# Kernel tuning notes

Hardware: AMD Instinct MI355X
Metric: run time of the kernel (lower is better)

Reference implementation:

```python
import jax, jax.numpy as jnp
import numpy as np

DIM_IN = 1024
DIM_Q = 1024
DIM_K = 1024
DIM_V = 1024
HEADS = 16

def setup_inputs() -> dict:
    key = jax.random.key(0)
    ks = jax.random.split(key, 5)
    s = 1.0 / np.sqrt(DIM_IN)
    return {
        "x": jax.random.normal(ks[0], (2, 2048, DIM_IN), dtype=jnp.float32),
        "Wq": jax.random.uniform(ks[1], (DIM_IN, DIM_Q), jnp.float32, -s, s),
        "Wk": jax.random.uniform(ks[2], (DIM_IN, DIM_K), jnp.float32, -s, s),
        "Wv": jax.random.uniform(ks[3], (DIM_IN, DIM_V), jnp.float32, -s, s),
        "Wo": jax.random.uniform(ks[4], (DIM_V, DIM_V), jnp.float32, -1.0/np.sqrt(DIM_V), 1.0/np.sqrt(DIM_V)),
    }

def reference(x, Wq, Wk, Wv, Wo):
    B, S, _ = x.shape
    H = HEADS
    q = (x @ Wq).reshape(B, S, H, DIM_Q // H).transpose(0, 2, 1, 3)  # [B,H,S,dq]
    k = (x @ Wk).reshape(B, S, H, DIM_K // H).transpose(0, 2, 1, 3)
    v = (x @ Wv).reshape(B, S, H, DIM_V // H).transpose(0, 2, 1, 3)
    scores = jnp.einsum("bhsd,bhtd->bhst", q, k)  # no pre-softmax scaling (as in source)
    # NOTE: source divides by sqrt(dim_q) AFTER softmax — replicated faithfully.
    attn = jax.nn.softmax(scores, axis=-1) / jnp.sqrt(jnp.float32(DIM_Q))
    out = jnp.einsum("bhst,bhtd->bhsd", attn, v)  # [B,H,S,dv]
    out = out.transpose(0, 2, 1, 3).reshape(B, S, DIM_V)
    return out @ Wo
```

## Files before the change

### kernel.cpp

```cpp
#include <hip/hip_runtime.h>
#include <hip/hip_bf16.h>


typedef __attribute__((ext_vector_type(8))) short bf16x8;
typedef __attribute__((ext_vector_type(4))) short short4v;
typedef __attribute__((ext_vector_type(4))) float f32x4;

typedef const __attribute__((address_space(1))) void gvoid_t;
typedef __attribute__((address_space(3))) void svoid_t;
#define GLDS16(g, l) \
  __builtin_amdgcn_global_load_lds((gvoid_t*)(g), (svoid_t*)(l), 16, 0, 0)

#define MFMA16(a, b, c) __builtin_amdgcn_mfma_f32_16x16x32_bf16((a), (b), (c), 0, 0, 0)

#if defined(__has_builtin)
#if __has_builtin(__builtin_amdgcn_exp2f)
#define EXP2(x) __builtin_amdgcn_exp2f(x)
#else
#define EXP2(x) exp2f(x)
#endif
#else
#define EXP2(x) exp2f(x)
#endif

#define LOG2E 1.4426950408889634f
#define NSHIFT 17.312340490667561f

static __device__ __forceinline__ short f2bf(float f) {
  __hip_bfloat16 h = __float2bfloat16(f);
  short s;
  __builtin_memcpy(&s, &h, 2);
  return s;
}

static __device__ __forceinline__ unsigned pack2bf(float lo, float hi) {
  float2 t; t.x = lo; t.y = hi;
  __hip_bfloat162 h2 = __float22bfloat162_rn(t);
  unsigned u;
  __builtin_memcpy(&u, &h2, 4);
  return u;
}

__global__ __launch_bounds__(256) void prep(const float* __restrict__ x,
                                            const float* __restrict__ Wq,
                                            const float* __restrict__ Wk,
                                            const float* __restrict__ Wv,
                                            const float* __restrict__ Wo,
                                            short* __restrict__ xb,
                                            short* __restrict__ wqkvt,
                                            short* __restrict__ wot) {
  __shared__ float tile[64][65];
  int bid = blockIdx.x;
  int tid = threadIdx.x;
  if (bid < 2048) {
    int i = bid * 256 + tid;
    const float4* p = (const float4*)(x + (size_t)i * 8);
    float4 a = p[0], b = p[1];
    bf16x8 o;
    o[0] = f2bf(a.x); o[1] = f2bf(a.y); o[2] = f2bf(a.z); o[3] = f2bf(a.w);
    o[4] = f2bf(b.x); o[5] = f2bf(b.y); o[6] = f2bf(b.z); o[7] = f2bf(b.w);
    *(bf16x8*)(xb + (size_t)i * 8) = o;
    return;
  }
  bid -= 2048;
  int mat = bid >> 8;
  int t = bid & 255;
  int tn = (t & 15) * 64;
  int tk = (t >> 4) * 64;
  const float* src = (mat == 0) ? Wq : (mat == 1) ? Wk : (mat == 2) ? Wv : Wo;
  short* dst = (mat < 3) ? (wqkvt + (size_t)mat * 1024 * 1024) : wot;

  int c4 = (tid & 15) * 4;
#pragma unroll
  for (int it = 0; it < 4; ++it) {
    int r = (tid >> 4) + it * 16;
    float4 v = *(const float4*)(src + (size_t)(tk + r) * 1024 + tn + c4);
    tile[r][c4 + 0] = v.x; tile[r][c4 + 1] = v.y;
    tile[r][c4 + 2] = v.z; tile[r][c4 + 3] = v.w;
  }
  __syncthreads();
  int n = tid >> 2;
  int kc = (tid & 3) * 16;
  bf16x8 o0, o1;
#pragma unroll
  for (int j = 0; j < 8; ++j) {
    o0[j] = f2bf(tile[kc + j][n]);
    o1[j] = f2bf(tile[kc + 8 + j][n]);
  }
  *(bf16x8*)(dst + (size_t)(tn + n) * 1024 + tk + kc) = o0;
  *(bf16x8*)(dst + (size_t)(tn + n) * 1024 + tk + kc + 8) = o1;
}

__global__ __launch_bounds__(512, 4) void gemm_qkv(const short* __restrict__ A,
                                                   const short* __restrict__ Bt,
                                                   short* __restrict__ qk,
                                                   short* __restrict__ vt) {
  constexpr int K = 1024;
  __shared__ short As[2][128 * 64];
  __shared__ short Bs[2][192 * 64];
  const int tid = threadIdx.x;
  const int lane = tid & 63;
  const int w = tid >> 6;
  const int lr = lane & 15, lg = lane >> 4;
  const int m0 = blockIdx.y * 128, n0 = blockIdx.x * 192;
  const int wm = (w >> 2) * 64, wn = (w & 3) * 48;

  auto stage = [&](int kt, int bb) {
#pragma unroll
    for (int it = 0; it < 2; ++it) {
      int id = it * 512 + tid;
      int row = id >> 3, c = id & 7;
      int sc = c ^ (row & 7);
      GLDS16(A + (size_t)(m0 + row) * K + kt + sc * 8, &As[bb][0] + id * 8);
    }
#pragma unroll
    for (int it = 0; it < 3; ++it) {
      int id = it * 512 + tid;
      int row = id >> 3, c = id & 7;
      int sc = c ^ (row & 7);
      GLDS16(Bt + (size_t)(n0 + row) * K + kt + sc * 8, &Bs[bb][0] + id * 8);
    }
  };

  f32x4 acc[4][3] = {};

  stage(0, 0);
  __syncthreads();

  int cur = 0;
  for (int kt = 0; kt < K; kt += 64) {
    if (kt + 64 < K) stage(kt + 64, cur ^ 1);
    const short* Ab = &As[cur][0];
    const short* Bb = &Bs[cur][0];
#pragma unroll
    for (int kk2 = 0; kk2 < 2; ++kk2) {
      int cw = kk2 * 4 + lg;
      bf16x8 bfr[3];
#pragma unroll
      for (int ni = 0; ni < 3; ++ni) {
        int row = wn + ni * 16 + lr;
        bfr[ni] = *(const bf16x8*)(Bb + row * 64 + ((cw ^ (row & 7)) * 8));
      }
      __builtin_amdgcn_s_setprio(1);
#pragma unroll
      for (int mi = 0; mi < 4; ++mi) {
        int row = wm + mi * 16 + lr;
        bf16x8 af = *(const bf16x8*)(Ab + row * 64 + ((cw ^ (row & 7)) * 8));
#pragma unroll
        for (int ni = 0; ni < 3; ++ni)
          acc[mi][ni] = MFMA16(af, bfr[ni], acc[mi][ni]);
      }
      __builtin_amdgcn_s_setprio(0);
    }
    __syncthreads();
    cur ^= 1;
  }

#pragma unroll
  for (int mi = 0; mi < 4; ++mi) {
#pragma unroll
    for (int ni = 0; ni < 3; ++ni) {
      int m = m0 + wm + mi * 16 + lg * 4;
      int n = n0 + wn + ni * 16 + lr;
      if (n < 2048) {
        float sc = (n < 1024) ? LOG2E : 1.0f;
#pragma unroll
        for (int r = 0; r < 4; ++r)
          qk[(size_t)(m + r) * 2048 + n] = f2bf(acc[mi][ni][r] * sc);
      } else {
        int nv = n - 2048;
        int vtrow = ((m >> 11) * 16 + (nv >> 6)) * 64 + (nv & 63);
        int scol = m & 2047;
        int psc = (scol & ~31) | ((scol & 0xC) << 1) | ((scol & 16) >> 2) |
                  (scol & 3);
        short4v pv;
#pragma unroll
        for (int r = 0; r < 4; ++r) pv[r] = f2bf(acc[mi][ni][r]);
        *(short4v*)(vt + (size_t)vtrow * 2048 + psc) = pv;
      }
    }
  }
}

__global__ __launch_bounds__(256) void gemm_out(const short* __restrict__ A,
                                                const short* __restrict__ Bt,
                                                float* __restrict__ C) {
  constexpr int K = 1024, N = 1024;
  __shared__ short As[2][128 * 64];
  __shared__ short Bs[2][64 * 64];
  const int tid = threadIdx.x;
  const int lane = tid & 63;
  const int w = tid >> 6;
  const int lr = lane & 15, lg = lane >> 4;
  const int m0 = blockIdx.y * 128, n0 = blockIdx.x * 64;
  const int wm = (w >> 1) * 64, wn = (w & 1) * 32;

  auto stage = [&](int kt, int bb) {
#pragma unroll
    for (int it = 0; it < 4; ++it) {
      int id = it * 256 + tid;
      int row = id >> 3, c = id & 7;
      int sc = c ^ (row & 7);
      GLDS16(A + (size_t)(m0 + row) * K + kt + sc * 8, &As[bb][0] + id * 8);
    }
#pragma unroll
    for (int it = 0; it < 2; ++it) {
      int id = it * 256 + tid;
      int row = id >> 3, c = id & 7;
      int sc = c ^ (row & 7);
      GLDS16(Bt + (size_t)(n0 + row) * K + kt + sc * 8, &Bs[bb][0] + id * 8);
    }
  };

  f32x4 acc[4][2] = {};

  stage(0, 0);
  __syncthreads();

  int cur = 0;
  for (int kt = 0; kt < K; kt += 64) {
    if (kt + 64 < K) stage(kt + 64, cur ^ 1);
    const short* Ab = &As[cur][0];
    const short* Bb = &Bs[cur][0];
#pragma unroll
    for (int kk2 = 0; kk2 < 2; ++kk2) {
      int cw = kk2 * 4 + lg;
      bf16x8 bfr[2];
#pragma unroll
      for (int ni = 0; ni < 2; ++ni) {
        int row = wn + ni * 16 + lr;
        bfr[ni] = *(const bf16x8*)(Bb + row * 64 + ((cw ^ (row & 7)) * 8));
      }
      __builtin_amdgcn_s_setprio(1);
#pragma unroll
      for (int mi = 0; mi < 4; ++mi) {
        int row = wm + mi * 16 + lr;
        bf16x8 af = *(const bf16x8*)(Ab + row * 64 + ((cw ^ (row & 7)) * 8));
#pragma unroll
        for (int ni = 0; ni < 2; ++ni)
          acc[mi][ni] = MFMA16(af, bfr[ni], acc[mi][ni]);
      }
      __builtin_amdgcn_s_setprio(0);
    }
    __syncthreads();
    cur ^= 1;
  }

#pragma unroll
  for (int mi = 0; mi < 4; ++mi) {
#pragma unroll
    for (int ni = 0; ni < 2; ++ni) {
      int m = m0 + wm + mi * 16 + lg * 4;
      int n = n0 + wn + ni * 16 + lr;
#pragma unroll
      for (int r = 0; r < 4; ++r) C[(size_t)(m + r) * N + n] = acc[mi][ni][r];
    }
  }
}

__global__ __launch_bounds__(256, 2) void attn_fwd(const short* __restrict__ qk,
                                                   const short* __restrict__ vt,
                                                   short* __restrict__ outb) {
  constexpr int S = 2048, LDQ = 2048;
  constexpr int NT = S / 128;
  const int fid = blockIdx.x;
  const int xcd = fid & 7, j = fid >> 3;
  const int qt = j & 15;
  const int pair = xcd * 4 + (j >> 4);
  const int h = pair & 15, b = pair >> 4;

  const int tid = threadIdx.x, lane = tid & 63, w = tid >> 6;
  const int lr = lane & 15, lg = lane >> 4;
  const int s7 = lr & 7;
  const int qb = qt * 128 + w * 32;

  __shared__ short Ks[2][128][64];
  __shared__ short Vs[2][64][128];

  const short* base = qk + (size_t)b * S * LDQ + h * 64;
  const short* vbase = vt + (size_t)(b * 16 + h) * 64 * 2048;

  bf16x8 qA0 = *(const bf16x8*)(base + (size_t)(qb + lr) * LDQ + lg * 8);
  bf16x8 qA1 = *(const bf16x8*)(base + (size_t)(qb + lr) * LDQ + 32 + lg * 8);
  bf16x8 qB0 = *(const bf16x8*)(base + (size_t)(qb + 16 + lr) * LDQ + lg * 8);
  bf16x8 qB1 = *(const bf16x8*)(base + (size_t)(qb + 16 + lr) * LDQ + 32 + lg * 8);

  bf16x8 ones;
#pragma unroll
  for (int i = 0; i < 8; ++i) ones[i] = (short)0x3F80;

  auto stageK = [&](int kt, int bb) {
#pragma unroll
    for (int it = 0; it < 4; ++it) {
      int id = it * 256 + tid;
      int row = id >> 3, c = id & 7;
      int sc = c ^ (row & 7);
      GLDS16(base + 1024 + (size_t)(kt + row) * LDQ + sc * 8,
             &Ks[bb][0][0] + id * 8);
    }
  };
  auto stageV = [&](int kt, int bb) {
#pragma unroll
    for (int it = 0; it < 4; ++it) {
      int id = it * 256 + tid;
      int row = id >> 4, c = id & 15;
      int sc = c ^ (row & 15);
      GLDS16(vbase + (size_t)row * 2048 + kt + sc * 8,
             &Vs[bb][0][0] + id * 8);
    }
  };

  f32x4 oA[4] = {}, oB[4] = {};
  f32x4 laccA = {}, laccB = {};
  bf16x8 pA[4], pB[4];

  stageK(0, 0);
  __syncthreads();

  for (int t = 0; t < NT; ++t) {
    const int cb = t & 1;
    if (t + 1 < NT) stageK((t + 1) * 128, cb ^ 1);
    stageV(t * 128, cb);

    const short* Kb = &Ks[cb][0][0];

    f32x4 sA[8], sB[8];
    __builtin_amdgcn_s_setprio(1);
#pragma unroll
    for (int kc = 0; kc < 8; ++kc) {
      int krow = kc * 16 + lr;
      bf16x8 kf0 = *(const bf16x8*)(Kb + krow * 64 + ((lg ^ s7) * 8));
      bf16x8 kf1 = *(const bf16x8*)(Kb + krow * 64 + (((4 + lg) ^ s7) * 8));
      f32x4 s = {-NSHIFT, -NSHIFT, -NSHIFT, -NSHIFT};
      s = MFMA16(kf0, qA0, s);
      s = MFMA16(kf1, qA1, s);
      sA[kc] = s;
      f32x4 u = {-NSHIFT, -NSHIFT, -NSHIFT, -NSHIFT};
      u = MFMA16(kf0, qB0, u);
      u = MFMA16(kf1, qB1, u);
      sB[kc] = u;
    }
    __builtin_amdgcn_s_setprio(0);

    if (t > 0) {
      const short* Vb = &Vs[cb ^ 1][0][0];
      __builtin_amdgcn_s_setprio(1);
#pragma unroll
      for (int g = 0; g < 4; ++g) {
        laccA = MFMA16(pA[g], ones, laccA);
        laccB = MFMA16(pB[g], ones, laccB);
      }
#pragma unroll
      for (int nc = 0; nc < 4; ++nc) {
        const short* vb = Vb + (nc * 16 + lr) * 128;
#pragma unroll
        for (int g = 0; g < 4; ++g) {
          bf16x8 vf = *(const bf16x8*)(vb + (((4 * g + lg) ^ lr) * 8));
          oA[nc] = MFMA16(pA[g], vf, oA[nc]);
          oB[nc] = MFMA16(pB[g], vf, oB[nc]);
        }
      }
      __builtin_amdgcn_s_setprio(0);
    }

    unsigned pwA[4][4], pwB[4][4];
#pragma unroll
    for (int kc = 0; kc < 8; ++kc) {
      {
        float p0 = EXP2(sA[kc][0]), p1 = EXP2(sA[kc][1]);
        float p2 = EXP2(sA[kc][2]), p3 = EXP2(sA[kc][3]);
        pwA[kc >> 1][(kc & 1) * 2 + 0] = pack2bf(p0, p1);
        pwA[kc >> 1][(kc & 1) * 2 + 1] = pack2bf(p2, p3);
      }
      {
        float p0 = EXP2(sB[kc][0]), p1 = EXP2(sB[kc][1]);
        float p2 = EXP2(sB[kc][2]), p3 = EXP2(sB[kc][3]);
        pwB[kc >> 1][(kc & 1) * 2 + 0] = pack2bf(p0, p1);
        pwB[kc >> 1][(kc & 1) * 2 + 1] = pack2bf(p2, p3);
      }
    }
#pragma unroll
    for (int g = 0; g < 4; ++g) {
      __builtin_memcpy(&pA[g], pwA[g], 16);
      __builtin_memcpy(&pB[g], pwB[g], 16);
    }

    __syncthreads();
  }

  {
    const short* Vb = &Vs[(NT - 1) & 1][0][0];
#pragma unroll
    for (int g = 0; g < 4; ++g) {
      laccA = MFMA16(pA[g], ones, laccA);
      laccB = MFMA16(pB[g], ones, laccB);
    }
#pragma unroll
    for (int nc = 0; nc < 4; ++nc) {
      const short* vb = Vb + (nc * 16 + lr) * 128;
#pragma unroll
      for (int g = 0; g < 4; ++g) {
        bf16x8 vf = *(const bf16x8*)(vb + (((4 * g + lg) ^ lr) * 8));
        oA[nc] = MFMA16(pA[g], vf, oA[nc]);
        oB[nc] = MFMA16(pB[g], vf, oB[nc]);
      }
    }
  }

#pragma unroll
  for (int r = 0; r < 4; ++r) {
    float dA = 1.0f / (laccA[r] * 32.0f);
    float dB = 1.0f / (laccB[r] * 32.0f);
#pragma unroll
    for (int nc = 0; nc < 4; ++nc) {
      int col = h * 64 + nc * 16 + lr;
      outb[(size_t)(b * S + qb + 4 * lg + r) * 1024 + col] = f2bf(oA[nc][r] * dA);
      outb[(size_t)(b * S + qb + 16 + 4 * lg + r) * 1024 + col] =
          f2bf(oB[nc][r] * dB);
    }
  }
}

extern "C" void kernel_launch(void* const* d_in, const int* in_sizes, int n_in,
                              void* d_out, int out_size, void* d_ws,
                              size_t ws_size, hipStream_t stream) {
  (void)in_sizes; (void)n_in; (void)out_size; (void)ws_size;
  const float* x = (const float*)d_in[0];
  const float* Wq = (const float*)d_in[1];
  const float* Wk = (const float*)d_in[2];
  const float* Wv = (const float*)d_in[3];
  const float* Wo = (const float*)d_in[4];

  char* p = (char*)d_ws;
  short* xb = (short*)p;      p += (size_t)4096 * 1024 * 2;
  short* wqkvt = (short*)p;   p += (size_t)3072 * 1024 * 2;
  short* wot = (short*)p;     p += (size_t)1024 * 1024 * 2;
  short* qk = (short*)p;      p += (size_t)4096 * 2048 * 2;
  short* vt = (short*)p;      p += (size_t)4096 * 1024 * 2;
  short* attno = (short*)p;   p += (size_t)4096 * 1024 * 2;

  prep<<<3072, 256, 0, stream>>>(x, Wq, Wk, Wv, Wo, xb, wqkvt, wot);
  gemm_qkv<<<dim3(16, 32), 512, 0, stream>>>(xb, wqkvt, qk, vt);
  attn_fwd<<<512, 256, 0, stream>>>(qk, vt, attno);
  gemm_out<<<dim3(16, 32), 256, 0, stream>>>(attno, wot, (float*)d_out);
}
```

Measured before the change: 102.8 us.

## Shrink attention tiles to 64 queries and 64 keys per block for more blocks

The attention kernel now gives each wave 16 query rows instead of 32 and uses 64-key tiles instead of 128. Launching 1024 blocks with a min-blocks-per-CU hint of 4 is meant to raise occupancy and parallelism, and it halves per-block LDS and register use. The cost is that each K/V tile is reused by fewer queries, so total K/V traffic doubles, and the loop runs twice as many iterations, each with a barrier.

```diff
diff --git a/kernel.cpp b/kernel.cpp
--- a/kernel.cpp
+++ b/kernel.cpp
@@ -258,32 +258,30 @@
   }
 }
 
-__global__ __launch_bounds__(256, 2) void attn_fwd(const short* __restrict__ qk,
+__global__ __launch_bounds__(256, 4) void attn_fwd(const short* __restrict__ qk,
                                                    const short* __restrict__ vt,
                                                    short* __restrict__ outb) {
   constexpr int S = 2048, LDQ = 2048;
-  constexpr int NT = S / 128;
+  constexpr int NT = S / 64;
   const int fid = blockIdx.x;
   const int xcd = fid & 7, j = fid >> 3;
-  const int qt = j & 15;
-  const int pair = xcd * 4 + (j >> 4);
+  const int qt = j & 31;
+  const int pair = xcd * 4 + (j >> 5);
   const int h = pair & 15, b = pair >> 4;
 
   const int tid = threadIdx.x, lane = tid & 63, w = tid >> 6;
   const int lr = lane & 15, lg = lane >> 4;
   const int s7 = lr & 7;
-  const int qb = qt * 128 + w * 32;
-
-  __shared__ short Ks[2][128][64];
-  __shared__ short Vs[2][64][128];
+  const int qb = qt * 64 + w * 16;
+
+  __shared__ short Ks[2][64][64];
+  __shared__ short Vs[2][64][64];
 
   const short* base = qk + (size_t)b * S * LDQ + h * 64;
   const short* vbase = vt + (size_t)(b * 16 + h) * 64 * 2048;
 
   bf16x8 qA0 = *(const bf16x8*)(base + (size_t)(qb + lr) * LDQ + lg * 8);
   bf16x8 qA1 = *(const bf16x8*)(base + (size_t)(qb + lr) * LDQ + 32 + lg * 8);
-  bf16x8 qB0 = *(const bf16x8*)(base + (size_t)(qb + 16 + lr) * LDQ + lg * 8);
-  bf16x8 qB1 = *(const bf16x8*)(base + (size_t)(qb + 16 + lr) * LDQ + 32 + lg * 8);
 
   bf16x8 ones;
 #pragma unroll
@@ -291,7 +289,7 @@
 
   auto stageK = [&](int kt, int bb) {
 #pragma unroll
-    for (int it = 0; it < 4; ++it) {
+    for (int it = 0; it < 2; ++it) {
       int id = it * 256 + tid;
       int row = id >> 3, c = id & 7;
       int sc = c ^ (row & 7);
@@ -301,33 +299,33 @@
   };
   auto stageV = [&](int kt, int bb) {
 #pragma unroll
-    for (int it = 0; it < 4; ++it) {
+    for (int it = 0; it < 2; ++it) {
       int id = it * 256 + tid;
-      int row = id >> 4, c = id & 15;
-      int sc = c ^ (row & 15);
+      int row = id >> 3, c = id & 7;
+      int sc = c ^ (row & 7);
       GLDS16(vbase + (size_t)row * 2048 + kt + sc * 8,
              &Vs[bb][0][0] + id * 8);
     }
   };
 
-  f32x4 oA[4] = {}, oB[4] = {};
-  f32x4 laccA = {}, laccB = {};
-  bf16x8 pA[4], pB[4];
+  f32x4 oA[4] = {};
+  f32x4 laccA = {};
+  bf16x8 pA[2];
 
   stageK(0, 0);
   __syncthreads();
 
   for (int t = 0; t < NT; ++t) {
     const int cb = t & 1;
-    if (t + 1 < NT) stageK((t + 1) * 128, cb ^ 1);
-    stageV(t * 128, cb);
+    if (t + 1 < NT) stageK((t + 1) * 64, cb ^ 1);
+    stageV(t * 64, cb);
 
     const short* Kb = &Ks[cb][0][0];
 
-    f32x4 sA[8], sB[8];
+    f32x4 sA[4];
     __builtin_amdgcn_s_setprio(1);
 #pragma unroll
-    for (int kc = 0; kc < 8; ++kc) {
+    for (int kc = 0; kc < 4; ++kc) {
       int krow = kc * 16 + lr;
       bf16x8 kf0 = *(const bf16x8*)(Kb + krow * 64 + ((lg ^ s7) * 8));
       bf16x8 kf1 = *(const bf16x8*)(Kb + krow * 64 + (((4 + lg) ^ s7) * 8));
@@ -335,10 +333,6 @@
       s = MFMA16(kf0, qA0, s);
       s = MFMA16(kf1, qA1, s);
       sA[kc] = s;
-      f32x4 u = {-NSHIFT, -NSHIFT, -NSHIFT, -NSHIFT};
-      u = MFMA16(kf0, qB0, u);
-      u = MFMA16(kf1, qB1, u);
-      sB[kc] = u;
     }
     __builtin_amdgcn_s_setprio(0);
 
@@ -346,44 +340,29 @@
       const short* Vb = &Vs[cb ^ 1][0][0];
       __builtin_amdgcn_s_setprio(1);
 #pragma unroll
-      for (int g = 0; g < 4; ++g) {
-        laccA = MFMA16(pA[g], ones, laccA);
-        laccB = MFMA16(pB[g], ones, laccB);
-      }
+      for (int g = 0; g < 2; ++g) laccA = MFMA16(pA[g], ones, laccA);
 #pragma unroll
       for (int nc = 0; nc < 4; ++nc) {
-        const short* vb = Vb + (nc * 16 + lr) * 128;
-#pragma unroll
-        for (int g = 0; g < 4; ++g) {
-          bf16x8 vf = *(const bf16x8*)(vb + (((4 * g + lg) ^ lr) * 8));
+        const short* vb = Vb + (nc * 16 + lr) * 64;
+#pragma unroll
+        for (int g = 0; g < 2; ++g) {
+          bf16x8 vf = *(const bf16x8*)(vb + (((4 * g + lg) ^ s7) * 8));
           oA[nc] = MFMA16(pA[g], vf, oA[nc]);
-          oB[nc] = MFMA16(pB[g], vf, oB[nc]);
         }
       }
       __builtin_amdgcn_s_setprio(0);
     }
 
-    unsigned pwA[4][4], pwB[4][4];
-#pragma unroll
-    for (int kc = 0; kc < 8; ++kc) {
-      {
-        float p0 = EXP2(sA[kc][0]), p1 = EXP2(sA[kc][1]);
-        float p2 = EXP2(sA[kc][2]), p3 = EXP2(sA[kc][3]);
-        pwA[kc >> 1][(kc & 1) * 2 + 0] = pack2bf(p0, p1);
-        pwA[kc >> 1][(kc & 1) * 2 + 1] = pack2bf(p2, p3);
-      }
-      {
-        float p0 = EXP2(sB[kc][0]), p1 = EXP2(sB[kc][1]);
-        float p2 = EXP2(sB[kc][2]), p3 = EXP2(sB[kc][3]);
-        pwB[kc >> 1][(kc & 1) * 2 + 0] = pack2bf(p0, p1);
-        pwB[kc >> 1][(kc & 1) * 2 + 1] = pack2bf(p2, p3);
-      }
-    }
-#pragma unroll
-    for (int g = 0; g < 4; ++g) {
-      __builtin_memcpy(&pA[g], pwA[g], 16);
-      __builtin_memcpy(&pB[g], pwB[g], 16);
-    }
+    unsigned pwA[2][4];
+#pragma unroll
+    for (int kc = 0; kc < 4; ++kc) {
+      float p0 = EXP2(sA[kc][0]), p1 = EXP2(sA[kc][1]);
+      float p2 = EXP2(sA[kc][2]), p3 = EXP2(sA[kc][3]);
+      pwA[kc >> 1][(kc & 1) * 2 + 0] = pack2bf(p0, p1);
+      pwA[kc >> 1][(kc & 1) * 2 + 1] = pack2bf(p2, p3);
+    }
+#pragma unroll
+    for (int g = 0; g < 2; ++g) __builtin_memcpy(&pA[g], pwA[g], 16);
 
     __syncthreads();
   }
@@ -391,18 +370,14 @@
   {
     const short* Vb = &Vs[(NT - 1) & 1][0][0];
 #pragma unroll
-    for (int g = 0; g < 4; ++g) {
-      laccA = MFMA16(pA[g], ones, laccA);
-      laccB = MFMA16(pB[g], ones, laccB);
-    }
+    for (int g = 0; g < 2; ++g) laccA = MFMA16(pA[g], ones, laccA);
 #pragma unroll
     for (int nc = 0; nc < 4; ++nc) {
-      const short* vb = Vb + (nc * 16 + lr) * 128;
-#pragma unroll
-      for (int g = 0; g < 4; ++g) {
-        bf16x8 vf = *(const bf16x8*)(vb + (((4 * g + lg) ^ lr) * 8));
+      const short* vb = Vb + (nc * 16 + lr) * 64;
+#pragma unroll
+      for (int g = 0; g < 2; ++g) {
+        bf16x8 vf = *(const bf16x8*)(vb + (((4 * g + lg) ^ s7) * 8));
         oA[nc] = MFMA16(pA[g], vf, oA[nc]);
-        oB[nc] = MFMA16(pB[g], vf, oB[nc]);
       }
     }
   }
@@ -410,13 +385,10 @@
 #pragma unroll
   for (int r = 0; r < 4; ++r) {
     float dA = 1.0f / (laccA[r] * 32.0f);
-    float dB = 1.0f / (laccB[r] * 32.0f);
 #pragma unroll
     for (int nc = 0; nc < 4; ++nc) {
       int col = h * 64 + nc * 16 + lr;
       outb[(size_t)(b * S + qb + 4 * lg + r) * 1024 + col] = f2bf(oA[nc][r] * dA);
-      outb[(size_t)(b * S + qb + 16 + 4 * lg + r) * 1024 + col] =
-          f2bf(oB[nc][r] * dB);
     }
   }
 }
@@ -441,6 +413,6 @@
 
   prep<<<3072, 256, 0, stream>>>(x, Wq, Wk, Wv, Wo, xb, wqkvt, wot);
   gemm_qkv<<<dim3(16, 32), 512, 0, stream>>>(xb, wqkvt, qk, vt);
-  attn_fwd<<<512, 256, 0, stream>>>(qk, vt, attno);
+  attn_fwd<<<1024, 256, 0, stream>>>(qk, vt, attno);
   gemm_out<<<dim3(16, 32), 256, 0, stream>>>(attno, wot, (float*)d_out);
 }
```

New measurement: 109.1 us. +6.1%, slower.
